# Kernel tuning notes

Hardware: AMD Instinct MI355X
Metric: run time of the kernel (lower is better)

The kernel has to match this reference:

```python
import jax, jax.numpy as jnp
import numpy as np

N_DRUG = 846
E = 256          # embedding_num
NS = 128         # neighbor_sample_size
N_ENT = 100000
N_REL = 200
BN_EPS = 1e-5


def setup_inputs() -> dict:
    key = jax.random.key(0)
    ks = jax.random.split(key, 12)
    return {
        "gnn1_embedding": jax.random.normal(ks[0], (N_DRUG, E), jnp.float32),
        "idx": 0,
        "drug_name": jnp.arange(N_DRUG, dtype=jnp.int64),
        "adj_tail": jax.random.randint(ks[1], (N_DRUG, NS), 0, N_ENT, dtype=jnp.int64),
        "adj_relation": jax.random.randint(ks[2], (N_DRUG, NS), 0, N_REL, dtype=jnp.int64),
        "drug_table": jax.random.normal(ks[3], (N_DRUG, E), jnp.float32),
        "rela_table": jax.random.normal(ks[4], (N_REL, E), jnp.float32),
        "ent_table": jax.random.normal(ks[5], (N_ENT, E), jnp.float32),
        "W1": jax.random.normal(ks[6], (N_DRUG, E, E), jnp.float32) * 0.05,
        "b1": jax.random.normal(ks[7], (NS, E), jnp.float32) * 0.05,
        "W2": jax.random.normal(ks[8], (N_DRUG, E, E), jnp.float32) * 0.05,
        "b2": jax.random.normal(ks[9], (NS, E), jnp.float32) * 0.05,
        "lin_w": jax.random.normal(ks[10], (2 * E, E), jnp.float32) * (1.0 / np.sqrt(2 * E)),
        "lin_b": jnp.zeros((E,), jnp.float32),
        "bn_gamma": jnp.ones((E,), jnp.float32),
        "bn_beta": jnp.zeros((E,), jnp.float32),
    }


def reference(gnn1_embedding, idx, drug_name, adj_tail, adj_relation,
              drug_table, rela_table, ent_table,
              W1, b1, W2, b2, lin_w, lin_b, bn_gamma, bn_beta):
    d = drug_table[drug_name]            # [846, E]
    r = rela_table[adj_relation]         # [846, NS, E]
    t = ent_table[adj_tail]              # [846, NS, E]

    dr = d[:, None, :] * r               # [846, NS, E]
    h = jnp.einsum('bne,bef->bnf', dr, W1) + b1   # per-drug batched matmul
    h = jax.nn.relu(h)
    h = jnp.einsum('bne,bef->bnf', h, W2) + b2
    score = jnp.sum(h, axis=-1)          # [846, NS]
    attn = jax.nn.softmax(score, axis=1) # softmax over neighbors

    weighted_ent = jnp.einsum('bn,bne->be', attn, t)   # [846, E]
    drug_e = jnp.concatenate([weighted_ent, d], axis=1)  # [846, 2E]

    x = drug_e @ lin_w + lin_b
    x = jax.nn.relu(x)
    # BatchNorm1d in training mode: biased batch stats over the drug axis
    mean = jnp.mean(x, axis=0)
    var = jnp.mean((x - mean) ** 2, axis=0)
    drug_f = (x - mean) * jax.lax.rsqrt(var + BN_EPS) * bn_gamma + bn_beta
    return (drug_f, gnn1_embedding, idx)
```

## Files before the change

kernel.cpp:

```cpp
#include <hip/hip_runtime.h>

#define NDRUG 846
#define EDIM 256
#define NS 128

typedef short s8v __attribute__((ext_vector_type(8)));
typedef __bf16 b8v __attribute__((ext_vector_type(8)));
typedef float f32x4 __attribute__((ext_vector_type(4)));

static __device__ __forceinline__ unsigned short f2bf(float f) {
  union { float f; unsigned u; } v; v.f = f;
  unsigned r = v.u + 0x7fffu + ((v.u >> 16) & 1u);
  return (unsigned short)(r >> 16);
}

template <typename V>
static __device__ __forceinline__ auto mfma_impl(V a, V b, f32x4 c, int)
    -> decltype(__builtin_amdgcn_mfma_f32_16x16x32_bf16(a, b, c, 0, 0, 0)) {
  return __builtin_amdgcn_mfma_f32_16x16x32_bf16(a, b, c, 0, 0, 0);
}
template <typename V>
static __device__ __forceinline__ f32x4 mfma_impl(V a, V b, f32x4 c, long) {
  b8v ab = __builtin_bit_cast(b8v, a);
  b8v bb = __builtin_bit_cast(b8v, b);
  return __builtin_amdgcn_mfma_f32_16x16x32_bf16(ab, bb, c, 0, 0, 0);
}
static __device__ __forceinline__ f32x4 mfma16(s8v a, s8v b, f32x4 c) {
  return mfma_impl(a, b, c, 0);
}

__global__ __launch_bounds__(512, 4) void gnn_main(
    const int* __restrict__ drug_name,
    const int* __restrict__ adj_tail,
    const int* __restrict__ adj_relation,
    const float* __restrict__ drug_table,
    const float* __restrict__ rela_table,
    const float* __restrict__ ent_table,
    const float* __restrict__ W1,
    const float* __restrict__ b1,
    const float* __restrict__ W2,
    const float* __restrict__ b2,
    const float* __restrict__ lin_w,
    const float* __restrict__ lin_b,
    float* __restrict__ xT) {
  __shared__ unsigned short s_ab[NS * EDIM];
  __shared__ float s_d[EDIM];
  __shared__ int s_tail[NS];
  __shared__ float s_w2sum[EDIM];
  __shared__ float s_b2sum[NS];
  __shared__ float s_scorep[8][NS];
  __shared__ float s_attn[NS];
  __shared__ float s_we[2][EDIM];
  __shared__ float s_lin[2][EDIM];

  const int b = blockIdx.x;
  const int tid = threadIdx.x;
  const int w = tid >> 6;
  const int l = tid & 63;
  const int g = l >> 4;
  const int lr = l & 15;

  if (tid < EDIM) {
    const int dn = drug_name[b];
    s_d[tid] = drug_table[(long)dn * EDIM + tid];
  } else if (tid < EDIM + NS) {
    s_tail[tid - EDIM] = adj_tail[b * NS + (tid - EDIM)];
  }

  {
    const int rg = tid >> 4;
    const int lc = (tid & 15) * 16;
    const float* W2p = W2 + (long)b * EDIM * EDIM;
#pragma unroll
    for (int s = 0; s < 8; ++s) {
      const int e = 32 * s + rg;
      const float* p = W2p + e * EDIM + lc;
      float4 a0 = *(const float4*)p, a1 = *(const float4*)(p + 4);
      float4 a2 = *(const float4*)(p + 8), a3 = *(const float4*)(p + 12);
      float v = a0.x + a0.y + a0.z + a0.w + a1.x + a1.y + a1.z + a1.w +
                a2.x + a2.y + a2.z + a2.w + a3.x + a3.y + a3.z + a3.w;
#pragma unroll
      for (int off = 1; off < 16; off <<= 1) v += __shfl_xor(v, off);
      if ((tid & 15) == 0) s_w2sum[e] = v;
    }
#pragma unroll
    for (int s = 0; s < 4; ++s) {
      const int n = 32 * s + rg;
      const float* p = b2 + n * EDIM + lc;
      float4 a0 = *(const float4*)p, a1 = *(const float4*)(p + 4);
      float4 a2 = *(const float4*)(p + 8), a3 = *(const float4*)(p + 12);
      float v = a0.x + a0.y + a0.z + a0.w + a1.x + a1.y + a1.z + a1.w +
                a2.x + a2.y + a2.z + a2.w + a3.x + a3.y + a3.z + a3.w;
#pragma unroll
      for (int off = 1; off < 16; off <<= 1) v += __shfl_xor(v, off);
      if ((tid & 15) == 0) s_b2sum[n] = v;
    }
  }
  __syncthreads();

  {
    const int n = tid >> 2;
    const int e0 = (tid & 3) * 64;
    const int rel = adj_relation[b * NS + n];
    const float* rrow = rela_table + (long)rel * EDIM;
    const int swz = (n & 7) << 4;
#pragma unroll
    for (int c = 0; c < 8; ++c) {
      const int e = e0 + c * 8;
      float4 p0 = *(const float4*)(rrow + e);
      float4 p1 = *(const float4*)(rrow + e + 4);
      s8v v;
      v[0] = (short)f2bf(p0.x * s_d[e + 0]);
      v[1] = (short)f2bf(p0.y * s_d[e + 1]);
      v[2] = (short)f2bf(p0.z * s_d[e + 2]);
      v[3] = (short)f2bf(p0.w * s_d[e + 3]);
      v[4] = (short)f2bf(p1.x * s_d[e + 4]);
      v[5] = (short)f2bf(p1.y * s_d[e + 5]);
      v[6] = (short)f2bf(p1.z * s_d[e + 6]);
      v[7] = (short)f2bf(p1.w * s_d[e + 7]);
      *(s8v*)((char*)s_ab + ((n * 512 + e * 2) ^ swz)) = v;
    }
  }
  __syncthreads();

  f32x4 acc[8][2];
#pragma unroll
  for (int mt = 0; mt < 8; ++mt) {
    acc[mt][0] = (f32x4){0.f, 0.f, 0.f, 0.f};
    acc[mt][1] = (f32x4){0.f, 0.f, 0.f, 0.f};
  }
  {
    const float* Wp = W1 + (long)b * EDIM * EDIM;
    const int col0 = 32 * w + lr;
    const int swz = (lr & 7) << 4;
    float fb[16];
    s8v bf0[2], bf1[2];
    {
      const float* pk = Wp + (8 * g) * EDIM + col0;
#pragma unroll
      for (int j = 0; j < 8; ++j) {
        fb[j] = pk[j * EDIM];
        fb[8 + j] = pk[j * EDIM + 16];
      }
#pragma unroll
      for (int j = 0; j < 8; ++j) {
        bf0[0][j] = (short)f2bf(fb[j]);
        bf1[0][j] = (short)f2bf(fb[8 + j]);
      }
    }
#pragma unroll
    for (int kk = 0; kk < 8; ++kk) {
      const int c = kk & 1;
      if (kk < 7) {
        const float* pk = Wp + (32 * (kk + 1) + 8 * g) * EDIM + col0;
#pragma unroll
        for (int j = 0; j < 8; ++j) {
          fb[j] = pk[j * EDIM];
          fb[8 + j] = pk[j * EDIM + 16];
        }
      }
      const int kb = (32 * kk + 8 * g) * 2;
#pragma unroll
      for (int mt = 0; mt < 8; ++mt) {
        const int row = 16 * mt + lr;
        s8v af = *(const s8v*)((const char*)s_ab + ((row * 512 + kb) ^ swz));
        acc[mt][0] = mfma16(af, bf0[c], acc[mt][0]);
        acc[mt][1] = mfma16(af, bf1[c], acc[mt][1]);
      }
      if (kk < 7) {
#pragma unroll
        for (int j = 0; j < 8; ++j) {
          bf0[c ^ 1][j] = (short)f2bf(fb[j]);
          bf1[c ^ 1][j] = (short)f2bf(fb[8 + j]);
        }
      }
    }
  }

#pragma unroll
  for (int mt = 0; mt < 8; ++mt) {
#pragma unroll
    for (int jj = 0; jj < 4; ++jj) {
      const int n = 16 * mt + 4 * g + jj;
      const int f0 = 32 * w + lr;
      const int f1 = f0 + 16;
      float v = fmaxf(acc[mt][0][jj] + b1[n * EDIM + f0], 0.f) * s_w2sum[f0] +
                fmaxf(acc[mt][1][jj] + b1[n * EDIM + f1], 0.f) * s_w2sum[f1];
#pragma unroll
      for (int off = 1; off < 16; off <<= 1) v += __shfl_xor(v, off);
      if (lr == 0) s_scorep[w][n] = v;
    }
  }
  __syncthreads();

  if (w == 0) {
    float v0 = s_b2sum[l], v1 = s_b2sum[l + 64];
#pragma unroll
    for (int ww = 0; ww < 8; ++ww) {
      v0 += s_scorep[ww][l];
      v1 += s_scorep[ww][l + 64];
    }
    float m = fmaxf(v0, v1);
#pragma unroll
    for (int off = 1; off < 64; off <<= 1) m = fmaxf(m, __shfl_xor(m, off));
    const float e0 = expf(v0 - m), e1 = expf(v1 - m);
    float s = e0 + e1;
#pragma unroll
    for (int off = 1; off < 64; off <<= 1) s += __shfl_xor(s, off);
    const float inv = 1.f / s;
    s_attn[l] = e0 * inv;
    s_attn[l + 64] = e1 * inv;
  }
  __syncthreads();

  {
    const int f = tid & 255;
    const int half = tid >> 8;
    const int nbase = half * 64;
    float a = 0.f;
#pragma unroll 8
    for (int i = 0; i < 64; ++i) {
      const int n = nbase + i;
      a += s_attn[n] * ent_table[(long)s_tail[n] * EDIM + f];
    }
    s_we[half][f] = a;
  }
  __syncthreads();

  {
    const int f = tid & 255;
    const int half = tid >> 8;
    const float* wp = lin_w + (long)half * EDIM * EDIM + f;
    float a = 0.f;
    if (half == 0) {
#pragma unroll 16
      for (int e = 0; e < EDIM; ++e) a += (s_we[0][e] + s_we[1][e]) * wp[(long)e * EDIM];
    } else {
#pragma unroll 16
      for (int e = 0; e < EDIM; ++e) a += s_d[e] * wp[(long)e * EDIM];
    }
    s_lin[half][f] = a;
  }
  __syncthreads();

  if (tid < EDIM) {
    float x = s_lin[0][tid] + s_lin[1][tid] + lin_b[tid];
    x = fmaxf(x, 0.f);
    xT[tid * NDRUG + b] = x;
  }
}

__global__ __launch_bounds__(256) void bn_kernel(const float* __restrict__ xT,
                                                 const float* __restrict__ gamma,
                                                 const float* __restrict__ beta,
                                                 float* __restrict__ out) {
  const int f = blockIdx.x;
  const int t = threadIdx.x;
  const float* col = xT + f * NDRUG;
  float s = 0.f, ss = 0.f;
  for (int i = t; i < NDRUG; i += 256) {
    const float v = col[i];
    s += v;
    ss += v * v;
  }
#pragma unroll
  for (int off = 1; off < 64; off <<= 1) {
    s += __shfl_xor(s, off);
    ss += __shfl_xor(ss, off);
  }
  __shared__ float as_[4], ass_[4];
  if ((t & 63) == 0) {
    as_[t >> 6] = s;
    ass_[t >> 6] = ss;
  }
  __syncthreads();
  s = as_[0] + as_[1] + as_[2] + as_[3];
  ss = ass_[0] + ass_[1] + ass_[2] + ass_[3];
  const float mean = s * (1.f / NDRUG);
  const float var = ss * (1.f / NDRUG) - mean * mean;
  const float sc = rsqrtf(var + 1e-5f) * gamma[f];
  const float sh = beta[f] - mean * sc;
  for (int i = t; i < NDRUG; i += 256) out[i * EDIM + f] = col[i] * sc + sh;
}

__global__ void tail_kernel(const float* __restrict__ gnn1, const int* __restrict__ idx,
                            float* __restrict__ out) {
  const int total4 = NDRUG * EDIM / 4;
  const float4* s4 = (const float4*)gnn1;
  float4* d4 = (float4*)(out + NDRUG * EDIM);
  for (int i = blockIdx.x * blockDim.x + threadIdx.x; i < total4;
       i += gridDim.x * blockDim.x)
    d4[i] = s4[i];
  if (blockIdx.x == 0 && threadIdx.x == 0) out[2 * NDRUG * EDIM] = (float)idx[0];
}

extern "C" void kernel_launch(void* const* d_in, const int* in_sizes, int n_in,
                              void* d_out, int out_size, void* d_ws, size_t ws_size,
                              hipStream_t stream) {
  const float* gnn1       = (const float*)d_in[0];
  const int*   idx        = (const int*)d_in[1];
  const int*   drug_name  = (const int*)d_in[2];
  const int*   adj_tail   = (const int*)d_in[3];
  const int*   adj_rel    = (const int*)d_in[4];
  const float* drug_table = (const float*)d_in[5];
  const float* rela_table = (const float*)d_in[6];
  const float* ent_table  = (const float*)d_in[7];
  const float* W1         = (const float*)d_in[8];
  const float* b1         = (const float*)d_in[9];
  const float* W2         = (const float*)d_in[10];
  const float* b2         = (const float*)d_in[11];
  const float* lin_w      = (const float*)d_in[12];
  const float* lin_b      = (const float*)d_in[13];
  const float* bn_g       = (const float*)d_in[14];
  const float* bn_b       = (const float*)d_in[15];

  float* out = (float*)d_out;
  float* xT  = (float*)d_ws;

  gnn_main<<<NDRUG, 512, 0, stream>>>(drug_name, adj_tail, adj_rel, drug_table,
                                      rela_table, ent_table, W1, b1, W2, b2,
                                      lin_w, lin_b, xT);
  bn_kernel<<<EDIM, 256, 0, stream>>>(xT, bn_g, bn_b, out);
  tail_kernel<<<240, 256, 0, stream>>>(gnn1, idx, out);
}
```

Before: 166.3 us.

## Deepen W1 prefetch, vectorize entity gather, reuse LDS and split linear accumulators

Replaces the manual bf16 rounding with the native __bf16 conversion. Double-buffers the fp32 W1 loads two k-steps ahead so global latency overlaps more MFMA work. Rewrites the attention-weighted entity gather to use float4 loads across 8 neighbor groups, adding a reduction pass through scratch space that reuses the s_ab LDS buffer. The final linear layer now uses four independent accumulators to shorten dependency chains. Together these add register pressure and one extra barrier.

```diff
diff --git a/kernel.cpp b/kernel.cpp
--- a/kernel.cpp
+++ b/kernel.cpp
@@ -1,4 +1,5 @@
 #include <hip/hip_runtime.h>
+#include <hip/hip_bf16.h>
 
 #define NDRUG 846
 #define EDIM 256
@@ -8,10 +9,9 @@
 typedef __bf16 b8v __attribute__((ext_vector_type(8)));
 typedef float f32x4 __attribute__((ext_vector_type(4)));
 
-static __device__ __forceinline__ unsigned short f2bf(float f) {
-  union { float f; unsigned u; } v; v.f = f;
-  unsigned r = v.u + 0x7fffu + ((v.u >> 16) & 1u);
-  return (unsigned short)(r >> 16);
+static __device__ __forceinline__ short bfs(float f) {
+  __bf16 h = (__bf16)f;
+  return __builtin_bit_cast(short, h);
 }
 
 template <typename V>
@@ -43,15 +43,13 @@
     const float* __restrict__ lin_w,
     const float* __restrict__ lin_b,
     float* __restrict__ xT) {
-  __shared__ unsigned short s_ab[NS * EDIM];
+  __shared__ __align__(16) unsigned short s_ab[NS * EDIM];
   __shared__ float s_d[EDIM];
   __shared__ int s_tail[NS];
   __shared__ float s_w2sum[EDIM];
   __shared__ float s_b2sum[NS];
   __shared__ float s_scorep[8][NS];
   __shared__ float s_attn[NS];
-  __shared__ float s_we[2][EDIM];
-  __shared__ float s_lin[2][EDIM];
 
   const int b = blockIdx.x;
   const int tid = threadIdx.x;
@@ -110,14 +108,14 @@
       float4 p0 = *(const float4*)(rrow + e);
       float4 p1 = *(const float4*)(rrow + e + 4);
       s8v v;
-      v[0] = (short)f2bf(p0.x * s_d[e + 0]);
-      v[1] = (short)f2bf(p0.y * s_d[e + 1]);
-      v[2] = (short)f2bf(p0.z * s_d[e + 2]);
-      v[3] = (short)f2bf(p0.w * s_d[e + 3]);
-      v[4] = (short)f2bf(p1.x * s_d[e + 4]);
-      v[5] = (short)f2bf(p1.y * s_d[e + 5]);
-      v[6] = (short)f2bf(p1.z * s_d[e + 6]);
-      v[7] = (short)f2bf(p1.w * s_d[e + 7]);
+      v[0] = bfs(p0.x * s_d[e + 0]);
+      v[1] = bfs(p0.y * s_d[e + 1]);
+      v[2] = bfs(p0.z * s_d[e + 2]);
+      v[3] = bfs(p0.w * s_d[e + 3]);
+      v[4] = bfs(p1.x * s_d[e + 4]);
+      v[5] = bfs(p1.y * s_d[e + 5]);
+      v[6] = bfs(p1.z * s_d[e + 6]);
+      v[7] = bfs(p1.w * s_d[e + 7]);
       *(s8v*)((char*)s_ab + ((n * 512 + e * 2) ^ swz)) = v;
     }
   }
@@ -133,48 +131,50 @@
     const float* Wp = W1 + (long)b * EDIM * EDIM;
     const int col0 = 32 * w + lr;
     const int swz = (lr & 7) << 4;
-    float fb[16];
+    float fb[2][16];
     s8v bf0[2], bf1[2];
-    {
-      const float* pk = Wp + (8 * g) * EDIM + col0;
-#pragma unroll
-      for (int j = 0; j < 8; ++j) {
-        fb[j] = pk[j * EDIM];
-        fb[8 + j] = pk[j * EDIM + 16];
-      }
-#pragma unroll
-      for (int j = 0; j < 8; ++j) {
-        bf0[0][j] = (short)f2bf(fb[j]);
-        bf1[0][j] = (short)f2bf(fb[8 + j]);
-      }
-    }
+
+#define LOADW(buf, kt)                                      \
+  do {                                                      \
+    const float* pk = Wp + ((kt)*32 + 8 * g) * EDIM + col0; \
+    _Pragma("unroll") for (int j = 0; j < 8; ++j) {         \
+      (buf)[j] = pk[j * EDIM];                              \
+      (buf)[8 + j] = pk[j * EDIM + 16];                     \
+    }                                                       \
+  } while (0)
+#define CVTW(d0, d1, src)                           \
+  do {                                              \
+    _Pragma("unroll") for (int j = 0; j < 8; ++j) { \
+      (d0)[j] = bfs((src)[j]);                      \
+      (d1)[j] = bfs((src)[8 + j]);                  \
+    }                                               \
+  } while (0)
+
+    LOADW(fb[0], 0);
+    LOADW(fb[1], 1);
+    CVTW(bf0[0], bf1[0], fb[0]);
+
 #pragma unroll
     for (int kk = 0; kk < 8; ++kk) {
       const int c = kk & 1;
-      if (kk < 7) {
-        const float* pk = Wp + (32 * (kk + 1) + 8 * g) * EDIM + col0;
-#pragma unroll
-        for (int j = 0; j < 8; ++j) {
-          fb[j] = pk[j * EDIM];
-          fb[8 + j] = pk[j * EDIM + 16];
-        }
-      }
+      if (kk + 2 < 8) LOADW(fb[c], kk + 2);
       const int kb = (32 * kk + 8 * g) * 2;
 #pragma unroll
       for (int mt = 0; mt < 8; ++mt) {
         const int row = 16 * mt + lr;
         s8v af = *(const s8v*)((const char*)s_ab + ((row * 512 + kb) ^ swz));
-        acc[mt][0] = mfma16(af, bf0[c], acc[mt][0]);
-        acc[mt][1] = mfma16(af, bf1[c], acc[mt][1]);
+        acc[mt][0] = mfma16(af, c ? bf0[1] : bf0[0], acc[mt][0]);
+        acc[mt][1] = mfma16(af, c ? bf1[1] : bf1[0], acc[mt][1]);
       }
-      if (kk < 7) {
-#pragma unroll
-        for (int j = 0; j < 8; ++j) {
-          bf0[c ^ 1][j] = (short)f2bf(fb[j]);
-          bf1[c ^ 1][j] = (short)f2bf(fb[8 + j]);
-        }
+      if (kk + 1 < 8) {
+        if (c)
+          CVTW(bf0[0], bf1[0], fb[0]);
+        else
+          CVTW(bf0[1], bf1[1], fb[1]);
       }
     }
+#undef LOADW
+#undef CVTW
   }
 
 #pragma unroll
@@ -213,17 +213,33 @@
   }
   __syncthreads();
 
-  {
-    const int f = tid & 255;
-    const int half = tid >> 8;
-    const int nbase = half * 64;
-    float a = 0.f;
+  float* s_scratch = (float*)s_ab;
+  float* s_we = (float*)s_ab + 2048;
+  float* s_lin = (float*)s_ab + 2304;
+
+  {
+    const int f4 = tid & 63;
+    const int ng = tid >> 6;
+    float4 a = {0.f, 0.f, 0.f, 0.f};
 #pragma unroll 8
-    for (int i = 0; i < 64; ++i) {
-      const int n = nbase + i;
-      a += s_attn[n] * ent_table[(long)s_tail[n] * EDIM + f];
-    }
-    s_we[half][f] = a;
+    for (int i = 0; i < 16; ++i) {
+      const int n = 16 * ng + i;
+      const float4 e4 = *(const float4*)(ent_table + (long)s_tail[n] * EDIM + 4 * f4);
+      const float at = s_attn[n];
+      a.x += at * e4.x;
+      a.y += at * e4.y;
+      a.z += at * e4.z;
+      a.w += at * e4.w;
+    }
+    *(float4*)(s_scratch + ng * 256 + 4 * f4) = a;
+  }
+  __syncthreads();
+
+  if (tid < EDIM) {
+    float v = 0.f;
+#pragma unroll
+    for (int ng = 0; ng < 8; ++ng) v += s_scratch[ng * 256 + tid];
+    s_we[tid] = v;
   }
   __syncthreads();
 
@@ -231,20 +247,21 @@
     const int f = tid & 255;
     const int half = tid >> 8;
     const float* wp = lin_w + (long)half * EDIM * EDIM + f;
-    float a = 0.f;
-    if (half == 0) {
-#pragma unroll 16
-      for (int e = 0; e < EDIM; ++e) a += (s_we[0][e] + s_we[1][e]) * wp[(long)e * EDIM];
-    } else {
-#pragma unroll 16
-      for (int e = 0; e < EDIM; ++e) a += s_d[e] * wp[(long)e * EDIM];
-    }
-    s_lin[half][f] = a;
+    const float* src = half ? s_d : s_we;
+    float a0 = 0.f, a1 = 0.f, a2 = 0.f, a3 = 0.f;
+#pragma unroll 8
+    for (int e = 0; e < 64; ++e) {
+      a0 += src[e] * wp[(long)e * EDIM];
+      a1 += src[e + 64] * wp[(long)(e + 64) * EDIM];
+      a2 += src[e + 128] * wp[(long)(e + 128) * EDIM];
+      a3 += src[e + 192] * wp[(long)(e + 192) * EDIM];
+    }
+    s_lin[half * EDIM + f] = (a0 + a1) + (a2 + a3);
   }
   __syncthreads();
 
   if (tid < EDIM) {
-    float x = s_lin[0][tid] + s_lin[1][tid] + lin_b[tid];
+    float x = s_lin[tid] + s_lin[EDIM + tid] + lin_b[tid];
     x = fmaxf(x, 0.f);
     xT[tid * NDRUG + b] = x;
   }
```

New measurement: 166.3 us. Within noise of the previous version (+0.0%).
